# Kernel optimization log

Measured on AMD Instinct MI355X. Metric: run time of the kernel, lower is better.

The kernel has to match this reference:

```python
import jax, jax.numpy as jnp
import numpy as np

TOPK = 2
ROUTED_SCALING_FACTOR = 1.0


def setup_inputs() -> dict:
    key = jax.random.key(0)
    k1, k2 = jax.random.split(key)
    N, D, E = 8192, 4096, 64
    x = jax.random.normal(k1, (N, D), dtype=jnp.float32)
    expert_embeddings = jax.random.normal(k2, (E, D), dtype=jnp.float32) * 0.02
    gate_bias = jnp.zeros((E,), dtype=jnp.float32)
    return {"x": x, "expert_embeddings": expert_embeddings, "gate_bias": gate_bias}


def reference(x, expert_embeddings, gate_bias):
    # logits: (N, E) = x @ W^T, computed in fp32 as in the original
    logits = jnp.einsum('nd,ed->ne', x.astype(jnp.float32), expert_embeddings.astype(jnp.float32))
    scores = jax.nn.sigmoid(logits)
    biased_scores = scores + gate_bias  # bias only affects expert selection
    _, indices = jax.lax.top_k(biased_scores, TOPK)  # (N, topk)
    weights = jnp.take_along_axis(scores, indices, axis=-1)  # gather unbiased scores
    weights = weights / jnp.sum(weights, axis=-1, keepdims=True)
    weights = weights * ROUTED_SCALING_FACTOR
    return weights, indices, scores
```

## Files before the change

kernel.cpp:

```cpp
#include <hip/hip_runtime.h>
#include <hip/hip_bf16.h>
#include <math.h>

#define NROWS 8192
#define DDIM  4096
#define NEXP  64
#define KSPLIT 8
#define KCHUNK (DDIM / KSPLIT)
#define KSTEPS (KCHUNK / 32)

typedef __attribute__((ext_vector_type(8))) short bf16x8;
typedef __attribute__((ext_vector_type(4))) float f32x4;

__device__ inline unsigned short bf16_rne(float f) {
    unsigned u = __builtin_bit_cast(unsigned, f);
    u += 0x7FFF + ((u >> 16) & 1);
    return (unsigned short)(u >> 16);
}

__device__ inline void split8(const float* xf, bf16x8& hi, bf16x8& lo) {
#pragma unroll
    for (int j = 0; j < 8; j++) {
        const unsigned short h = bf16_rne(xf[j]);
        const float hf = __builtin_bit_cast(float, (unsigned)h << 16);
        hi[j] = (short)h;
        lo[j] = (short)bf16_rne(xf[j] - hf);
    }
}

__global__ __launch_bounds__(256) void wfrag_kernel(
    const float* __restrict__ w, unsigned short* __restrict__ whi,
    unsigned short* __restrict__ wlo)
{
    const int kc = blockIdx.x;
    const int t  = threadIdx.x >> 6;
    const int l  = threadIdx.x & 63;
    const int e  = t * 16 + (l & 15);
    const int k0 = kc * 32 + ((l >> 4) * 8);
    const float* p = w + (size_t)e * DDIM + k0;
    float xf[8];
    *(float4*)&xf[0] = *(const float4*)p;
    *(float4*)&xf[4] = *(const float4*)(p + 4);
    bf16x8 hi, lo;
    split8(xf, hi, lo);
    const size_t off = ((size_t)(kc * 4 + t) * 64 + l) * 8;
    *(bf16x8*)(whi + off) = hi;
    *(bf16x8*)(wlo + off) = lo;
}

__global__ __launch_bounds__(256) void gemm_partial_kernel(
    const float* __restrict__ x, const unsigned short* __restrict__ whi,
    const unsigned short* __restrict__ wlo, float* __restrict__ part)
{
    const int tid = threadIdx.x;
    const int wv  = tid >> 6;
    const int l   = tid & 63;
    const int q   = l >> 4;
    const int r0  = blockIdx.x * 64 + wv * 16;
    const int kh  = blockIdx.y;
    const int kb  = kh * KCHUNK;

    const float* xp = x + (size_t)(r0 + (l & 15)) * DDIM + kb + q * 8;
    const unsigned short* bhp = whi + ((size_t)(kb / 32) * 4 * 64 + l) * 8;
    const unsigned short* blp = wlo + ((size_t)(kb / 32) * 4 * 64 + l) * 8;

    f32x4 acc[4] = {f32x4{0,0,0,0}, f32x4{0,0,0,0}, f32x4{0,0,0,0}, f32x4{0,0,0,0}};

    float  xf[2][8];
    bf16x8 bh[2][4], bl[2][4];

    *(float4*)&xf[0][0] = *(const float4*)(xp);
    *(float4*)&xf[0][4] = *(const float4*)(xp + 4);
#pragma unroll
    for (int t = 0; t < 4; t++) {
        bh[0][t] = *(const bf16x8*)(bhp + (size_t)t * 64 * 8);
        bl[0][t] = *(const bf16x8*)(blp + (size_t)t * 64 * 8);
    }

    for (int s = 0; s < KSTEPS; s++) {
        const int cur = s & 1, nxt = cur ^ 1;
        if (s + 1 < KSTEPS) {
            const float* xpn = xp + (s + 1) * 32;
            const unsigned short* bhn = bhp + (size_t)(s + 1) * 4 * 64 * 8;
            const unsigned short* bln = blp + (size_t)(s + 1) * 4 * 64 * 8;
            *(float4*)&xf[nxt][0] = *(const float4*)(xpn);
            *(float4*)&xf[nxt][4] = *(const float4*)(xpn + 4);
#pragma unroll
            for (int t = 0; t < 4; t++) {
                bh[nxt][t] = *(const bf16x8*)(bhn + (size_t)t * 64 * 8);
                bl[nxt][t] = *(const bf16x8*)(bln + (size_t)t * 64 * 8);
            }
        }
        bf16x8 ahi, alo;
        split8(xf[cur], ahi, alo);
#pragma unroll
        for (int t = 0; t < 4; t++) {
            acc[t] = __builtin_amdgcn_mfma_f32_16x16x32_bf16(ahi, bh[cur][t], acc[t], 0, 0, 0);
            acc[t] = __builtin_amdgcn_mfma_f32_16x16x32_bf16(ahi, bl[cur][t], acc[t], 0, 0, 0);
            acc[t] = __builtin_amdgcn_mfma_f32_16x16x32_bf16(alo, bh[cur][t], acc[t], 0, 0, 0);
        }
    }

    float* po = part + (size_t)kh * NROWS * NEXP;
#pragma unroll
    for (int t = 0; t < 4; t++)
#pragma unroll
        for (int r = 0; r < 4; r++)
            po[(size_t)(r0 + q * 4 + r) * NEXP + t * 16 + (l & 15)] = acc[t][r];
}

__global__ __launch_bounds__(256) void gate_topk_kernel(
    const float* __restrict__ part, const float* __restrict__ bias,
    float* __restrict__ out)
{
    const int tid = threadIdx.x;
    const int e   = tid & 63;
    const int row = blockIdx.x * 4 + (tid >> 6);
    const size_t idx = (size_t)row * NEXP + e;

    float logit = 0.f;
#pragma unroll
    for (int s = 0; s < KSPLIT; s++)
        logit += part[(size_t)s * NROWS * NEXP + idx];
    const float score = 1.0f / (1.0f + expf(-logit));
    out[(size_t)4 * NROWS + idx] = score;

    const float biased = score + bias[e];

    float v = biased; int bi = e;
#pragma unroll
    for (int off = 32; off; off >>= 1) {
        const float ov = __shfl_xor(v, off);
        const int   oi = __shfl_xor(bi, off);
        if (ov > v || (ov == v && oi < bi)) { v = ov; bi = oi; }
    }
    const int i1 = bi;

    float v2 = (e == i1) ? -INFINITY : biased;
    int bi2 = e;
#pragma unroll
    for (int off = 32; off; off >>= 1) {
        const float ov = __shfl_xor(v2, off);
        const int   oi = __shfl_xor(bi2, off);
        if (ov > v2 || (ov == v2 && oi < bi2)) { v2 = ov; bi2 = oi; }
    }
    const int i2 = bi2;

    const float s1 = __shfl(score, i1);
    const float s2 = __shfl(score, i2);
    if (e == 0) {
        const float inv = 1.0f / (s1 + s2);
        out[(size_t)row * 2 + 0] = s1 * inv;
        out[(size_t)row * 2 + 1] = s2 * inv;
        out[(size_t)2 * NROWS + row * 2 + 0] = (float)i1;
        out[(size_t)2 * NROWS + row * 2 + 1] = (float)i2;
    }
}

extern "C" void kernel_launch(void* const* d_in, const int* in_sizes, int n_in,
                              void* d_out, int out_size, void* d_ws, size_t ws_size,
                              hipStream_t stream)
{
    const float* x    = (const float*)d_in[0];
    const float* w    = (const float*)d_in[1];
    const float* bias = (const float*)d_in[2];
    float* out  = (float*)d_out;

    float* part = (float*)d_ws;
    const size_t part_bytes = (size_t)KSPLIT * NROWS * NEXP * 4;
    unsigned short* whi = (unsigned short*)((char*)d_ws + part_bytes);
    unsigned short* wlo = (unsigned short*)((char*)d_ws + part_bytes + (size_t)NEXP * DDIM * 2);

    wfrag_kernel<<<DDIM / 32, 256, 0, stream>>>(w, whi, wlo);
    dim3 g1(NROWS / 64, KSPLIT);
    gemm_partial_kernel<<<g1, 256, 0, stream>>>(x, whi, wlo, part);
    gate_topk_kernel<<<NROWS / 4, 256, 0, stream>>>(part, bias, out);
}
```

Before: 221.5 us.

## Give each wave two row tiles to reuse W fragments, adapt K-split to workspace

Each wave now computes 32 rows instead of 16, so every W hi/lo fragment load feeds two MFMA row tiles. W fragments are no longer double-buffered; only the x tile is prefetched. K-split becomes a runtime value, up to 16, reduced until the partials fit in the workspace, which keeps the grid size at 64x16 blocks. This halves W traffic per row but doubles the partial-sum buffer the reduction kernel must read, and its sum loop is no longer unrolled.

```diff
diff --git a/kernel.cpp b/kernel.cpp
--- a/kernel.cpp
+++ b/kernel.cpp
@@ -5,9 +5,6 @@
 #define NROWS 8192
 #define DDIM  4096
 #define NEXP  64
-#define KSPLIT 8
-#define KCHUNK (DDIM / KSPLIT)
-#define KSTEPS (KCHUNK / 32)
 
 typedef __attribute__((ext_vector_type(8))) short bf16x8;
 typedef __attribute__((ext_vector_type(4))) float f32x4;
@@ -50,68 +47,86 @@
 
 __global__ __launch_bounds__(256) void gemm_partial_kernel(
     const float* __restrict__ x, const unsigned short* __restrict__ whi,
-    const unsigned short* __restrict__ wlo, float* __restrict__ part)
+    const unsigned short* __restrict__ wlo, float* __restrict__ part,
+    int ksplit)
 {
     const int tid = threadIdx.x;
     const int wv  = tid >> 6;
     const int l   = tid & 63;
     const int q   = l >> 4;
-    const int r0  = blockIdx.x * 64 + wv * 16;
+    const int col = l & 15;
+    const int r0  = blockIdx.x * 128 + wv * 32;
     const int kh  = blockIdx.y;
-    const int kb  = kh * KCHUNK;
+    const int kchunk = DDIM / ksplit;
+    const int ksteps = kchunk / 32;
+    const int kb  = kh * kchunk;
 
-    const float* xp = x + (size_t)(r0 + (l & 15)) * DDIM + kb + q * 8;
+    const float* xp0 = x + (size_t)(r0 + col) * DDIM + kb + q * 8;
+    const float* xp1 = xp0 + (size_t)16 * DDIM;
     const unsigned short* bhp = whi + ((size_t)(kb / 32) * 4 * 64 + l) * 8;
     const unsigned short* blp = wlo + ((size_t)(kb / 32) * 4 * 64 + l) * 8;
 
-    f32x4 acc[4] = {f32x4{0,0,0,0}, f32x4{0,0,0,0}, f32x4{0,0,0,0}, f32x4{0,0,0,0}};
+    f32x4 acc[2][4];
+#pragma unroll
+    for (int m = 0; m < 2; m++)
+#pragma unroll
+        for (int t = 0; t < 4; t++) acc[m][t] = f32x4{0, 0, 0, 0};
 
-    float  xf[2][8];
-    bf16x8 bh[2][4], bl[2][4];
+    float xf[2][2][8];
 
-    *(float4*)&xf[0][0] = *(const float4*)(xp);
-    *(float4*)&xf[0][4] = *(const float4*)(xp + 4);
+    *(float4*)&xf[0][0][0] = *(const float4*)(xp0);
+    *(float4*)&xf[0][0][4] = *(const float4*)(xp0 + 4);
+    *(float4*)&xf[0][1][0] = *(const float4*)(xp1);
+    *(float4*)&xf[0][1][4] = *(const float4*)(xp1 + 4);
+
+    for (int s = 0; s < ksteps; s++) {
+        const int cur = s & 1, nxt = cur ^ 1;
+
+        bf16x8 bh[4], bl[4];
+        const unsigned short* bhs = bhp + (size_t)s * 4 * 64 * 8;
+        const unsigned short* bls = blp + (size_t)s * 4 * 64 * 8;
 #pragma unroll
-    for (int t = 0; t < 4; t++) {
-        bh[0][t] = *(const bf16x8*)(bhp + (size_t)t * 64 * 8);
-        bl[0][t] = *(const bf16x8*)(blp + (size_t)t * 64 * 8);
-    }
+        for (int t = 0; t < 4; t++) {
+            bh[t] = *(const bf16x8*)(bhs + (size_t)t * 64 * 8);
+            bl[t] = *(const bf16x8*)(bls + (size_t)t * 64 * 8);
+        }
 
-    for (int s = 0; s < KSTEPS; s++) {
-        const int cur = s & 1, nxt = cur ^ 1;
-        if (s + 1 < KSTEPS) {
-            const float* xpn = xp + (s + 1) * 32;
-            const unsigned short* bhn = bhp + (size_t)(s + 1) * 4 * 64 * 8;
-            const unsigned short* bln = blp + (size_t)(s + 1) * 4 * 64 * 8;
-            *(float4*)&xf[nxt][0] = *(const float4*)(xpn);
-            *(float4*)&xf[nxt][4] = *(const float4*)(xpn + 4);
+        if (s + 1 < ksteps) {
+            const float* xn0 = xp0 + (s + 1) * 32;
+            const float* xn1 = xp1 + (s + 1) * 32;
+            *(float4*)&xf[nxt][0][0] = *(const float4*)(xn0);
+            *(float4*)&xf[nxt][0][4] = *(const float4*)(xn0 + 4);
+            *(float4*)&xf[nxt][1][0] = *(const float4*)(xn1);
+            *(float4*)&xf[nxt][1][4] = *(const float4*)(xn1 + 4);
+        }
+
+        bf16x8 ah[2], al[2];
+        split8(xf[cur][0], ah[0], al[0]);
+        split8(xf[cur][1], ah[1], al[1]);
+#pragma unroll
+        for (int m = 0; m < 2; m++)
 #pragma unroll
             for (int t = 0; t < 4; t++) {
-                bh[nxt][t] = *(const bf16x8*)(bhn + (size_t)t * 64 * 8);
-                bl[nxt][t] = *(const bf16x8*)(bln + (size_t)t * 64 * 8);
+                acc[m][t] = __builtin_amdgcn_mfma_f32_16x16x32_bf16(ah[m], bh[t], acc[m][t], 0, 0, 0);
+                acc[m][t] = __builtin_amdgcn_mfma_f32_16x16x32_bf16(ah[m], bl[t], acc[m][t], 0, 0, 0);
+                acc[m][t] = __builtin_amdgcn_mfma_f32_16x16x32_bf16(al[m], bh[t], acc[m][t], 0, 0, 0);
             }
-        }
-        bf16x8 ahi, alo;
-        split8(xf[cur], ahi, alo);
-#pragma unroll
-        for (int t = 0; t < 4; t++) {
-            acc[t] = __builtin_amdgcn_mfma_f32_16x16x32_bf16(ahi, bh[cur][t], acc[t], 0, 0, 0);
-            acc[t] = __builtin_amdgcn_mfma_f32_16x16x32_bf16(ahi, bl[cur][t], acc[t], 0, 0, 0);
-            acc[t] = __builtin_amdgcn_mfma_f32_16x16x32_bf16(alo, bh[cur][t], acc[t], 0, 0, 0);
-        }
     }
 
     float* po = part + (size_t)kh * NROWS * NEXP;
 #pragma unroll
-    for (int t = 0; t < 4; t++)
+    for (int m = 0; m < 2; m++)
 #pragma unroll
-        for (int r = 0; r < 4; r++)
-            po[(size_t)(r0 + q * 4 + r) * NEXP + t * 16 + (l & 15)] = acc[t][r];
+        for (int t = 0; t < 4; t++)
+#pragma unroll
+            for (int r = 0; r < 4; r++)
+                po[(size_t)(r0 + m * 16 + q * 4 + r) * NEXP + t * 16 + col] =
+                    acc[m][t][r];
 }
 
 __global__ __launch_bounds__(256) void gate_topk_kernel(
     const float* __restrict__ part, const float* __restrict__ bias,
-    float* __restrict__ out)
+    float* __restrict__ out, int ksplit)
 {
     const int tid = threadIdx.x;
     const int e   = tid & 63;
@@ -119,8 +134,7 @@
     const size_t idx = (size_t)row * NEXP + e;
 
     float logit = 0.f;
-#pragma unroll
-    for (int s = 0; s < KSPLIT; s++)
+    for (int s = 0; s < ksplit; s++)
         logit += part[(size_t)s * NROWS * NEXP + idx];
     const float score = 1.0f / (1.0f + expf(-logit));
     out[(size_t)4 * NROWS + idx] = score;
@@ -166,13 +180,18 @@
     const float* bias = (const float*)d_in[2];
     float* out  = (float*)d_out;
 
+    int ksplit = 16;
+    const size_t wbytes = (size_t)NEXP * DDIM * 2 * 2;
+    while (ksplit > 1 &&
+           (size_t)ksplit * NROWS * NEXP * 4 + wbytes > ws_size) ksplit >>= 1;
+
     float* part = (float*)d_ws;
-    const size_t part_bytes = (size_t)KSPLIT * NROWS * NEXP * 4;
+    const size_t part_bytes = (size_t)ksplit * NROWS * NEXP * 4;
     unsigned short* whi = (unsigned short*)((char*)d_ws + part_bytes);
-    unsigned short* wlo = (unsigned short*)((char*)d_ws + part_bytes + (size_t)NEXP * DDIM * 2);
+    unsigned short* wlo = whi + (size_t)NEXP * DDIM;
 
     wfrag_kernel<<<DDIM / 32, 256, 0, stream>>>(w, whi, wlo);
-    dim3 g1(NROWS / 64, KSPLIT);
-    gemm_partial_kernel<<<g1, 256, 0, stream>>>(x, whi, wlo, part);
-    gate_topk_kernel<<<NROWS / 4, 256, 0, stream>>>(part, bias, out);
+    dim3 g1(NROWS / 128, ksplit);
+    gemm_partial_kernel<<<g1, 256, 0, stream>>>(x, whi, wlo, part, ksplit);
+    gate_topk_kernel<<<NROWS / 4, 256, 0, stream>>>(part, bias, out, ksplit);
 }
```

Result: slower. 251.7 us (+13.6%).
